# Kernel optimization log

Measured on AMD Instinct MI355X. Metric: run time of the kernel, lower is better.

## Reference

```python
import jax, jax.numpy as jnp
import numpy as np

B, N_PROP = 2, 512
C_FEAT, FH, FW = 256, 200, 200
NUM_CLASSES, NUM_STAGES = 81, 3
POOL, SR, SCALE = 7, 2, 0.25
IMG_H, IMG_W = 800.0, 800.0
FC_DIM = 1024
IN_DIM = C_FEAT * POOL * POOL
STDS = ((0.1, 0.1, 0.2, 0.2), (0.05, 0.05, 0.1, 0.1), (0.033, 0.033, 0.067, 0.067))
CLIP_VAL = float(np.log(1000.0 / 16))
SCORE_T, NMS_T, DETS, PRE_NMS = 0.05, 0.5, 100, 2048


def bilinear(f, y, x):
    # f: [C,H,W]; y,x: [M] sample coords (torchvision roi_align bilinear rules)
    H, W = f.shape[1], f.shape[2]
    valid = (y > -1.0) & (y < H) & (x > -1.0) & (x < W)
    y = jnp.clip(y, 0.0, H - 1.0)
    x = jnp.clip(x, 0.0, W - 1.0)
    y0 = jnp.floor(y).astype(jnp.int32)
    x0 = jnp.floor(x).astype(jnp.int32)
    y1 = jnp.minimum(y0 + 1, H - 1)
    x1 = jnp.minimum(x0 + 1, W - 1)
    ly, lx = y - y0, x - x0
    hy, hx = 1.0 - ly, 1.0 - lx
    v = (hy * hx) * f[:, y0, x0] + (hy * lx) * f[:, y0, x1] \
      + (ly * hx) * f[:, y1, x0] + (ly * lx) * f[:, y1, x1]
    return v * valid  # [C,M]


def roi_align(f, rois):
    # f: [C,H,W], rois: [N,4] image coords -> [N,C,POOL,POOL]
    b = rois * SCALE
    x1, y1, x2, y2 = b[:, 0], b[:, 1], b[:, 2], b[:, 3]
    rw = jnp.maximum(x2 - x1, 1.0)
    rh = jnp.maximum(y2 - y1, 1.0)
    bw, bh = rw / POOL, rh / POOL
    p = jnp.arange(POOL, dtype=f.dtype)
    s = (jnp.arange(SR, dtype=f.dtype) + 0.5) / SR
    gy = y1[:, None, None] + (p[None, :, None] + s[None, None, :]) * bh[:, None, None]  # [N,P,SR]
    gx = x1[:, None, None] + (p[None, :, None] + s[None, None, :]) * bw[:, None, None]
    n = rois.shape[0]
    yy = jnp.broadcast_to(gy[:, :, :, None, None], (n, POOL, SR, POOL, SR))
    xx = jnp.broadcast_to(gx[:, None, None, :, :], (n, POOL, SR, POOL, SR))
    vals = bilinear(f, yy.reshape(-1), xx.reshape(-1))  # [C, N*P*SR*P*SR]
    vals = vals.reshape(f.shape[0], n, POOL, SR, POOL, SR).mean(axis=(3, 5))
    return vals.transpose(1, 0, 2, 3)


def decode_clip(props, deltas, stds):
    px1, py1, px2, py2 = props[:, 0], props[:, 1], props[:, 2], props[:, 3]
    pw = jnp.maximum(px2 - px1, 1e-6)
    ph = jnp.maximum(py2 - py1, 1e-6)
    px = px1 + 0.5 * pw
    py = py1 + 0.5 * ph
    wx, wy, ww, wh = stds
    dx = deltas[:, 0] * wx
    dy = deltas[:, 1] * wy
    dw = jnp.minimum(deltas[:, 2] * ww, CLIP_VAL)
    dh = jnp.minimum(deltas[:, 3] * wh, CLIP_VAL)
    gx = dx * pw + px
    gy = dy * ph + py
    gw = jnp.exp(dw) * pw
    gh = jnp.exp(dh) * ph
    return jnp.stack([jnp.clip(gx - 0.5 * gw, 0.0, IMG_W),
                      jnp.clip(gy - 0.5 * gh, 0.0, IMG_H),
                      jnp.clip(gx + 0.5 * gw, 0.0, IMG_W),
                      jnp.clip(gy + 0.5 * gh, 0.0, IMG_H)], axis=1)


def box_iou(a, b):
    area_a = (a[:, 2] - a[:, 0]) * (a[:, 3] - a[:, 1])
    area_b = (b[:, 2] - b[:, 0]) * (b[:, 3] - b[:, 1])
    lt = jnp.maximum(a[:, None, :2], b[None, :, :2])
    rb = jnp.minimum(a[:, None, 2:], b[None, :, 2:])
    wh = jnp.maximum(rb - lt, 0.0)
    inter = wh[..., 0] * wh[..., 1]
    return inter / (area_a[:, None] + area_b[None, :] - inter + 1e-12)


def postprocess(boxes, probs):
    # boxes [N,4], probs [N,NUM_CLASSES] -> fixed-size padded detections
    n = boxes.shape[0]
    ws = boxes[:, 2] - boxes[:, 0]
    hs = boxes[:, 3] - boxes[:, 1]
    ok = (ws >= 1.0) & (hs >= 1.0)  # remove_small_boxes(min_size=1.0)
    fg = probs[:, 1:]               # drop background (class 0)
    sc = jnp.where((fg > SCORE_T) & ok[:, None], fg, -1.0).reshape(-1)  # [N*(C-1)]
    labels = jnp.broadcast_to(jnp.arange(1, NUM_CLASSES, dtype=jnp.int32)[None, :],
                              (n, NUM_CLASSES - 1)).reshape(-1)
    bflat = jnp.broadcast_to(boxes[:, None, :], (n, NUM_CLASSES - 1, 4)).reshape(-1, 4)
    vals, idx = jax.lax.top_k(sc, PRE_NMS)  # fixed-size candidate cap, sorted desc
    bsel = bflat[idx]
    lsel = labels[idx]
    # batched_nms trick: offset boxes per label so classes never overlap
    off = bsel + (lsel.astype(bsel.dtype) * (jnp.max(bsel) + 1.0))[:, None]
    iou = box_iou(off, off)
    valid = vals > 0.0
    ar = jnp.arange(PRE_NMS)
    def body(i, keep):
        sup = (iou[i] > NMS_T) & keep[i]
        return keep & ~(sup & (ar > i))
    keep = jax.lax.fori_loop(0, PRE_NMS, body, valid)
    order = jnp.argsort(jnp.where(keep, ar, PRE_NMS + ar))[:DETS]  # kept first, score order
    kv = keep[order]
    out_boxes = jnp.where(kv[:, None], bsel[order], 0.0)
    out_scores = jnp.where(kv, vals[order], 0.0)
    out_labels = jnp.where(kv, lsel[order], 0)
    return out_boxes, out_scores, out_labels


def cascade_forward(features, proposals, W1, b1, W2, b2, Wc, bc, Wr, br):
    cur = proposals  # [B,N,4]
    logits = None
    for s in range(NUM_STAGES):
        pooled = jax.vmap(roi_align)(features, cur)  # [B,N,C,P,P]
        x = pooled.reshape(B * N_PROP, IN_DIM)
        h = jax.nn.relu(x @ W1[s] + b1[s])
        h = jax.nn.relu(h @ W2[s] + b2[s])
        logits = h @ Wc[s] + bc[s]
        deltas = (h @ Wr[s] + br[s]).reshape(B, N_PROP, 4)
        stds = STDS[s]
        cur = jax.vmap(lambda p, d: decode_clip(p, d, stds))(cur, deltas)
    probs = jax.nn.softmax(logits, axis=-1).reshape(B, N_PROP, NUM_CLASSES)
    return jax.vmap(postprocess)(cur, probs)


def setup_inputs() -> dict:
    key = jax.random.key(0)
    ks = jax.random.split(key, 12)
    features = jax.random.normal(ks[0], (B, C_FEAT, FH, FW), jnp.float32)
    cx = jax.random.uniform(ks[1], (B, N_PROP), minval=0.0, maxval=IMG_W)
    cy = jax.random.uniform(ks[2], (B, N_PROP), minval=0.0, maxval=IMG_H)
    w = jax.random.uniform(ks[3], (B, N_PROP), minval=16.0, maxval=256.0)
    h = jax.random.uniform(ks[4], (B, N_PROP), minval=16.0, maxval=256.0)
    proposals = jnp.stack([jnp.clip(cx - w / 2, 0.0, IMG_W), jnp.clip(cy - h / 2, 0.0, IMG_H),
                           jnp.clip(cx + w / 2, 0.0, IMG_W), jnp.clip(cy + h / 2, 0.0, IMG_H)],
                          axis=-1)
    def lin(k, fan_in, shape):
        return jax.random.normal(k, shape, jnp.float32) / np.sqrt(fan_in).astype(np.float32)
    W1 = lin(ks[5], IN_DIM, (NUM_STAGES, IN_DIM, FC_DIM))
    W2 = lin(ks[6], FC_DIM, (NUM_STAGES, FC_DIM, FC_DIM))
    Wc = lin(ks[7], FC_DIM, (NUM_STAGES, FC_DIM, NUM_CLASSES))
    Wr = lin(ks[8], FC_DIM, (NUM_STAGES, FC_DIM, 4)) * 0.5
    b1 = jnp.zeros((NUM_STAGES, FC_DIM), jnp.float32)
    b2 = jnp.zeros((NUM_STAGES, FC_DIM), jnp.float32)
    bc = jnp.zeros((NUM_STAGES, NUM_CLASSES), jnp.float32)
    br = jnp.zeros((NUM_STAGES, 4), jnp.float32)
    return {"features": features, "proposals": proposals, "W1": W1, "b1": b1,
            "W2": W2, "b2": b2, "Wc": Wc, "bc": bc, "Wr": Wr, "br": br}


def reference(features, proposals, W1, b1, W2, b2, Wc, bc, Wr, br):
    return cascade_forward(features, proposals, W1, b1, W2, b2, Wc, bc, Wr, br)
```

## Files before the change

### kernel.cpp

```cpp
#include <hip/hip_runtime.h>
#include <float.h>
#include <math.h>

#define NB 2
#define NPROP 512
#define NROI 1024
#define CFEAT 256
#define FH 200
#define FW 200
#define HWSZ 40000
#define INDIM 12544
#define FCD 1024
#define NCLS 81
#define NCAND 40960
#define CAP 4096
#define NSEL 2048
#define DETS 100
#define CLIPV 4.135166556742356f

#define KKT1 392
#define KKT2 32
#define SPLITK 8

typedef __attribute__((ext_vector_type(8))) short short8v;
typedef __attribute__((ext_vector_type(8))) unsigned short ushort8v;
typedef __attribute__((ext_vector_type(4))) float float4v;

__device__ __forceinline__ unsigned short f2bf(float x) {
    unsigned u = __float_as_uint(x);
    unsigned r = (u + 0x7fffu + ((u >> 16) & 1u)) >> 16;
    return (unsigned short)r;
}
__device__ __forceinline__ float bf2f(unsigned short b) {
    return __uint_as_float(((unsigned)b) << 16);
}
__device__ __forceinline__ void split3(float x, unsigned short& h, unsigned short& m, unsigned short& l) {
    h = f2bf(x);
    float r1 = x - bf2f(h);
    m = f2bf(r1);
    float r2 = r1 - bf2f(m);
    l = f2bf(r2);
}

__device__ __forceinline__ void gload_lds16(const void* g, void* l) {
    __builtin_amdgcn_global_load_lds((const __attribute__((address_space(1))) unsigned int*)g,
                                     (__attribute__((address_space(3))) unsigned int*)l, 16, 0, 0);
}

__device__ __forceinline__ int swz8k(int o) {
    return o ^ ((((o >> 6) ^ (o >> 8)) & 3) << 4);
}

__global__ void zero_ints_k(int* p, int n) {
    int i = blockIdx.x * blockDim.x + threadIdx.x;
    if (i < n) p[i] = 0;
}

__global__ __launch_bounds__(256) void transpose_k(const float* __restrict__ in, float* __restrict__ out) {
    __shared__ float tile[32][33];
    int b = blockIdx.z;
    int hw0 = blockIdx.x * 32;
    int c0 = blockIdx.y * 32;
    int tx = threadIdx.x;
    int ty = threadIdx.y;
#pragma unroll
    for (int i = 0; i < 32; i += 8)
        tile[ty + i][tx] = in[((size_t)(b * CFEAT + c0 + ty + i)) * HWSZ + hw0 + tx];
    __syncthreads();
#pragma unroll
    for (int i = 0; i < 32; i += 8)
        out[((size_t)b * HWSZ + hw0 + ty + i) * CFEAT + c0 + tx] = tile[tx][ty + i];
}

template<bool TRANS>
__device__ __forceinline__ float bil_sample(const float* __restrict__ feat, int b, int c,
                                            float yy, float xx) {
    bool valid = (yy > -1.f) && (yy < (float)FH) && (xx > -1.f) && (xx < (float)FW);
    float yc = fminf(fmaxf(yy, 0.f), (float)(FH - 1));
    float xc = fminf(fmaxf(xx, 0.f), (float)(FW - 1));
    int y0 = (int)floorf(yc), x0 = (int)floorf(xc);
    int y1i = min(y0 + 1, FH - 1), x1i = min(x0 + 1, FW - 1);
    float ly = yc - (float)y0, lx = xc - (float)x0;
    float hy = 1.f - ly, hx = 1.f - lx;
    float v00, v01, v10, v11;
    if (TRANS) {
        const float* base = feat + (size_t)b * HWSZ * CFEAT;
        v00 = base[((size_t)(y0 * FW + x0)) * CFEAT + c];
        v01 = base[((size_t)(y0 * FW + x1i)) * CFEAT + c];
        v10 = base[((size_t)(y1i * FW + x0)) * CFEAT + c];
        v11 = base[((size_t)(y1i * FW + x1i)) * CFEAT + c];
    } else {
        const float* base = feat + ((size_t)(b * CFEAT + c)) * HWSZ;
        v00 = base[y0 * FW + x0];
        v01 = base[y0 * FW + x1i];
        v10 = base[y1i * FW + x0];
        v11 = base[y1i * FW + x1i];
    }
    float v = hy * hx * v00 + hy * lx * v01 + ly * hx * v10 + ly * lx * v11;
    return valid ? v : 0.f;
}

template<bool TRANS>
__global__ __launch_bounds__(256) void roi_k(const float* __restrict__ feat,
                                             const float* __restrict__ boxes,
                                             float* __restrict__ xout) {
    int pp = blockIdx.x, r = blockIdx.y, c = threadIdx.x;
    int b = r >> 9;
    const float* bx = boxes + (size_t)r * 4;
    float x1 = bx[0] * 0.25f, y1 = bx[1] * 0.25f, x2 = bx[2] * 0.25f, y2 = bx[3] * 0.25f;
    float rw = fmaxf(x2 - x1, 1.0f), rh = fmaxf(y2 - y1, 1.0f);
    float bw = rw / 7.0f, bh = rh / 7.0f;
    int py = pp / 7, px = pp % 7;
    float acc = 0.f;
#pragma unroll
    for (int sy = 0; sy < 2; ++sy)
#pragma unroll
        for (int sx = 0; sx < 2; ++sx)
            acc += bil_sample<TRANS>(feat, b, c,
                                     y1 + ((float)py + 0.25f + 0.5f * (float)sy) * bh,
                                     x1 + ((float)px + 0.25f + 0.5f * (float)sx) * bw);
    xout[(size_t)r * INDIM + pp * 256 + c] = acc * 0.25f;
}

__global__ __launch_bounds__(256) void roi_split4_k(const float* __restrict__ feat,
                                                    const float* __restrict__ boxes,
                                                    unsigned short* __restrict__ Ap) {
    int tid = threadIdx.x;
    int g = tid >> 7;
    int binhalf = (tid >> 6) & 1;
    int cl = tid & 63;
    int r = blockIdx.x * 2 + g;
    int b = r >> 9;
    const float* bx = boxes + (size_t)r * 4;
    float x1 = bx[0] * 0.25f, y1 = bx[1] * 0.25f, x2 = bx[2] * 0.25f, y2 = bx[3] * 0.25f;
    float rw = fmaxf(x2 - x1, 1.0f), rh = fmaxf(y2 - y1, 1.0f);
    float bw = rw / 7.0f, bh = rh / 7.0f;
    int mt = r >> 7, rr = r & 127;
    size_t pstr = (size_t)8 * KKT1 * 4096;
    const float* base = feat + (size_t)b * HWSZ * CFEAT;
    for (int pp = binhalf; pp < 49; pp += 2) {
        int py = pp / 7, px = pp % 7;
        float ax = 0.f, ay = 0.f, az = 0.f, aw = 0.f;
#pragma unroll
        for (int sy = 0; sy < 2; ++sy) {
#pragma unroll
            for (int sx = 0; sx < 2; ++sx) {
                float yy = y1 + ((float)py + 0.25f + 0.5f * (float)sy) * bh;
                float xx = x1 + ((float)px + 0.25f + 0.5f * (float)sx) * bw;
                bool valid = (yy > -1.f) && (yy < (float)FH) && (xx > -1.f) && (xx < (float)FW);
                float yc = fminf(fmaxf(yy, 0.f), (float)(FH - 1));
                float xc = fminf(fmaxf(xx, 0.f), (float)(FW - 1));
                int y0 = (int)floorf(yc), x0 = (int)floorf(xc);
                int y1i = min(y0 + 1, FH - 1), x1i = min(x0 + 1, FW - 1);
                float ly = yc - (float)y0, lx = xc - (float)x0;
                float hy = 1.f - ly, hx = 1.f - lx;
                float w00 = hy * hx, w01 = hy * lx, w10 = ly * hx, w11 = ly * lx;
                if (!valid) { w00 = w01 = w10 = w11 = 0.f; }
                float4 v00 = ((const float4*)(base + (size_t)(y0 * FW + x0) * CFEAT))[cl];
                float4 v01 = ((const float4*)(base + (size_t)(y0 * FW + x1i) * CFEAT))[cl];
                float4 v10 = ((const float4*)(base + (size_t)(y1i * FW + x0) * CFEAT))[cl];
                float4 v11 = ((const float4*)(base + (size_t)(y1i * FW + x1i) * CFEAT))[cl];
                ax += w00 * v00.x + w01 * v01.x + w10 * v10.x + w11 * v11.x;
                ay += w00 * v00.y + w01 * v01.y + w10 * v10.y + w11 * v11.y;
                az += w00 * v00.z + w01 * v01.z + w10 * v10.z + w11 * v11.z;
                aw += w00 * v00.w + w01 * v01.w + w10 * v10.w + w11 * v11.w;
            }
        }
        ax *= 0.25f; ay *= 0.25f; az *= 0.25f; aw *= 0.25f;
        ushort4 h4, m4, l4;
        split3(ax, h4.x, m4.x, l4.x);
        split3(ay, h4.y, m4.y, l4.y);
        split3(az, h4.z, m4.z, l4.z);
        split3(aw, h4.w, m4.w, l4.w);
        int k0 = pp * 256 + cl * 4;
        int kk = k0 >> 5;
        size_t tile = ((size_t)mt * KKT1 + kk) * 4096 + rr * 32 + (k0 & 31);
        *(ushort4*)&Ap[tile] = h4;
        *(ushort4*)&Ap[tile + pstr] = m4;
        *(ushort4*)&Ap[tile + 2 * pstr] = l4;
    }
}

template<bool PERM>
__global__ __launch_bounds__(256) void wsplit_k(const float* __restrict__ W,
                                                unsigned short* __restrict__ out, int kkT) {
    __shared__ float tf[32][132];
    int nt = blockIdx.x, kk = blockIdx.y;
    int t = threadIdx.x;
    int kloc = t >> 3;
    int f4 = t & 7;
    int krow;
    if (PERM) krow = ((kk & 7) * 32 + kloc) * 49 + (kk >> 3);
    else krow = kk * 32 + kloc;
    const float* src = W + (size_t)krow * 1024 + nt * 128;
#pragma unroll
    for (int q = 0; q < 4; ++q) {
        float4 v = *(const float4*)(src + (f4 + q * 8) * 4);
        *(float4*)&tf[kloc][(f4 + q * 8) * 4] = v;
    }
    __syncthreads();
    int r = t >> 1;
    size_t tileBase = ((size_t)nt * kkT + kk) * 4096;
    size_t pstr = (size_t)8 * kkT * 4096;
#pragma unroll
    for (int cc = 0; cc < 2; ++cc) {
        int c = (t & 1) * 2 + cc;
        ushort8v hv, mv, lv;
#pragma unroll
        for (int e = 0; e < 8; ++e) {
            unsigned short h, m, l;
            split3(tf[c * 8 + e][r], h, m, l);
            hv[e] = h; mv[e] = m; lv[e] = l;
        }
        size_t o = tileBase + r * 32 + c * 8;
        *(ushort8v*)&out[o] = hv;
        *(ushort8v*)&out[o + pstr] = mv;
        *(ushort8v*)&out[o + 2 * pstr] = lv;
    }
}

__global__ __launch_bounds__(256) void wsplit_head_k(const float* __restrict__ Wc,
                                                     const float* __restrict__ Wr,
                                                     unsigned short* __restrict__ out) {
    int kk = blockIdx.x, t = threadIdx.x;
    int r = t >> 1;
    int k0 = (t & 1) * 16;
    size_t pstr = (size_t)KKT2 * 4096;
    for (int e = 0; e < 16; ++e) {
        int k = k0 + e;
        int krow = kk * 32 + k;
        float v = 0.f;
        if (r < 81) v = Wc[(size_t)krow * 81 + r];
        else if (r < 85) v = Wr[(size_t)krow * 4 + (r - 81)];
        unsigned short h, m, l;
        split3(v, h, m, l);
        size_t o = (size_t)kk * 4096 + r * 32 + k;
        out[o] = h;
        out[o + pstr] = m;
        out[o + 2 * pstr] = l;
    }
}

#define TERM16(AF) { _Pragma("unroll") for (int i = 0; i < 4; ++i) _Pragma("unroll") \
    for (int j = 0; j < 4; ++j) acc[i][j] = __builtin_amdgcn_mfma_f32_16x16x32_bf16(AF[i], bf[j], acc[i][j], 0, 0, 0); }

__global__ __launch_bounds__(256) void gemm_mfma_k(const unsigned short* __restrict__ Ap,
                                                   const unsigned short* __restrict__ Bp,
                                                   float* __restrict__ partial,
                                                   int kkT, int kkPer, int NT, int N) {
    __shared__ unsigned short sA[3][4096];
    __shared__ unsigned short sB[2][3][4096];
    int tid = threadIdx.x;
    int phys = blockIdx.x;
    int logical = (phys & 7) * (gridDim.x >> 3) + (phys >> 3);
    int tpc = 8 * NT;
    int xy = logical % tpc;
    int ck = logical / tpc;
    int mt = xy & 7, nt = xy >> 3;
    int kk0 = ck * kkPer;
    size_t pstrA = (size_t)8 * kkT * 4096 * 2;
    size_t pstrB = (size_t)NT * kkT * 4096 * 2;
    const char* aBase = (const char*)(Ap + (size_t)mt * kkT * 4096);
    const char* bBase = (const char*)(Bp + (size_t)nt * kkT * 4096);

    float4v acc[4][4];
#pragma unroll
    for (int i = 0; i < 4; ++i)
#pragma unroll
        for (int j = 0; j < 4; ++j) acc[i][j] = (float4v){0.f, 0.f, 0.f, 0.f};

    int lane = tid & 63, wv = tid >> 6;
    int wr = wv >> 1, wc = wv & 1;
    int ln = lane & 15;
    int q = lane >> 4;
    int qs = (q ^ (ln ^ (ln >> 2))) & 3;
    int aoffE = (wr * 64 + ln) * 32 + qs * 8;
    int boffE = (wc * 64 + ln) * 32 + qs * 8;

    int o0 = tid * 16;
    int o1 = o0 + 4096;
    int s0 = swz8k(o0);
    int s1 = swz8k(o1);

    auto stageA = [&](int kk) {
        const char* at = aBase + (size_t)kk * 8192;
#pragma unroll
        for (int p = 0; p < 3; ++p) {
            gload_lds16(at + (size_t)p * pstrA + s0, (char*)sA[p] + o0);
            gload_lds16(at + (size_t)p * pstrA + s1, (char*)sA[p] + o1);
        }
    };
    auto stageB = [&](int buf, int kk) {
        const char* bt = bBase + (size_t)kk * 8192;
#pragma unroll
        for (int p = 0; p < 3; ++p) {
            gload_lds16(bt + (size_t)p * pstrB + s0, (char*)sB[buf][p] + o0);
            gload_lds16(bt + (size_t)p * pstrB + s1, (char*)sB[buf][p] + o1);
        }
    };

    stageB(0, kk0);
    for (int it = 0; it < kkPer; ++it) {
        int cur = it & 1;
        stageA(kk0 + it);
        if (it + 1 < kkPer) {
            stageB(cur ^ 1, kk0 + it + 1);
            asm volatile("s_waitcnt vmcnt(6)" ::: "memory");
        } else {
            asm volatile("s_waitcnt vmcnt(0)" ::: "memory");
        }
        __builtin_amdgcn_s_barrier();
        __builtin_amdgcn_sched_barrier(0);
        short8v af[3][4];
#pragma unroll
        for (int p = 0; p < 3; ++p)
#pragma unroll
            for (int f = 0; f < 4; ++f)
                af[p][f] = *(const short8v*)&sA[p][aoffE + f * 512];
        short8v bf[4];
#pragma unroll
        for (int f = 0; f < 4; ++f) bf[f] = *(const short8v*)&sB[cur][0][boffE + f * 512];
        TERM16(af[0]); TERM16(af[1]); TERM16(af[2]);
#pragma unroll
        for (int f = 0; f < 4; ++f) bf[f] = *(const short8v*)&sB[cur][1][boffE + f * 512];
        TERM16(af[0]); TERM16(af[1]);
#pragma unroll
        for (int f = 0; f < 4; ++f) bf[f] = *(const short8v*)&sB[cur][2][boffE + f * 512];
        TERM16(af[0]);
        __builtin_amdgcn_sched_barrier(0);
        __builtin_amdgcn_s_barrier();
    }
    float* outp = partial + (size_t)ck * 1024 * N;
    int row0 = mt * 128 + wr * 64 + (lane >> 4) * 4;
    int col = nt * 128 + wc * 64 + ln;
#pragma unroll
    for (int i = 0; i < 4; ++i)
#pragma unroll
        for (int j = 0; j < 4; ++j)
#pragma unroll
            for (int qq = 0; qq < 4; ++qq)
                outp[(size_t)(row0 + i * 16 + qq) * N + col + j * 16] = acc[i][j][qq];
}

template<int NS>
__global__ void reduce8_k(const float* __restrict__ partial, const float* __restrict__ bias,
                          unsigned short* __restrict__ planes) {
    int i = blockIdx.x * 256 + threadIdx.x;
    float s = 0.f;
#pragma unroll
    for (int c = 0; c < NS; ++c) s += partial[((size_t)c << 20) + i];
    s += bias[i & 1023];
    s = fmaxf(s, 0.f);
    int m = i >> 10, n = i & 1023;
    int mt = m >> 7, rr = m & 127, kk = n >> 5;
    unsigned short h, mm_, l;
    split3(s, h, mm_, l);
    size_t tile = ((size_t)mt * KKT2 + kk) * 4096 + rr * 32 + (n & 31);
    size_t pstr = (size_t)8 * KKT2 * 4096;
    planes[tile] = h;
    planes[tile + pstr] = mm_;
    planes[tile + 2 * pstr] = l;
}

__global__ __launch_bounds__(128) void head_dec_k(const float* __restrict__ partial,
                                                  const float* __restrict__ bc,
                                                  const float* __restrict__ br,
                                                  const float* __restrict__ prev,
                                                  float* __restrict__ logits,
                                                  float* __restrict__ nxt,
                                                  float wx, float wy, float ww, float wh,
                                                  int write_logits) {
    int m = blockIdx.x;
    int tid = threadIdx.x;
    __shared__ float dl[4];
    if (tid < 85) {
        float s = 0.f;
#pragma unroll
        for (int c = 0; c < 8; ++c) s += partial[(size_t)c * 131072 + m * 128 + tid];
        if (tid < 81) {
            if (write_logits) logits[(size_t)m * NCLS + tid] = s + bc[tid];
        } else {
            dl[tid - 81] = s + br[tid - 81];
        }
    }
    __syncthreads();
    if (tid == 0) {
        const float* p = prev + (size_t)m * 4;
        float px1 = p[0], py1 = p[1], px2 = p[2], py2 = p[3];
        float pw = fmaxf(px2 - px1, 1e-6f), ph = fmaxf(py2 - py1, 1e-6f);
        float pcx = px1 + 0.5f * pw, pcy = py1 + 0.5f * ph;
        float dx = dl[0] * wx, dy = dl[1] * wy;
        float dw = fminf(dl[2] * ww, CLIPV);
        float dh = fminf(dl[3] * wh, CLIPV);
        float gx = dx * pw + pcx, gy = dy * ph + pcy;
        float gw = expf(dw) * pw, gh = expf(dh) * ph;
        nxt[(size_t)m * 4 + 0] = fminf(fmaxf(gx - 0.5f * gw, 0.f), 800.f);
        nxt[(size_t)m * 4 + 1] = fminf(fmaxf(gy - 0.5f * gh, 0.f), 800.f);
        nxt[(size_t)m * 4 + 2] = fminf(fmaxf(gx + 0.5f * gw, 0.f), 800.f);
        nxt[(size_t)m * 4 + 3] = fminf(fmaxf(gy + 0.5f * gh, 0.f), 800.f);
    }
}

template<bool PERM>
__global__ __launch_bounds__(256) void gemm_k(const float* __restrict__ A,
                                              const float* __restrict__ Bm,
                                              float* __restrict__ partial,
                                              int K_total, int Kchunk) {
    const int M = 1024, N = 1024;
    __shared__ float As[2][16][128];
    __shared__ float Bs[2][16][64];
    int tid = threadIdx.x;
    int mb = blockIdx.x & 7;
    int nb = blockIdx.x >> 3;
    int ck = blockIdx.y;
    int k0 = ck * Kchunk;
    int am = tid >> 1;
    int ak = (tid & 1) * 8;
    int bk = tid >> 4;
    int bn = (tid & 15) * 4;
    int ty = tid >> 4, tx = tid & 15;
    const float* Aptr = A + (size_t)(mb * 128 + am) * K_total + k0 + ak;

    float acc[8][4];
#pragma unroll
    for (int i = 0; i < 8; ++i)
#pragma unroll
        for (int j = 0; j < 4; ++j) acc[i][j] = 0.f;

    auto bRowPtr = [&](int kk) -> const float* {
        int row = PERM ? ((kk & 255) * 49 + (kk >> 8)) : kk;
        return Bm + (size_t)row * N + nb * 64 + bn;
    };

    int T = Kchunk / 16;
    float4 a0 = *(const float4*)(Aptr);
    float4 a1 = *(const float4*)(Aptr + 4);
    float4 b0 = *(const float4*)bRowPtr(k0 + bk);
    As[0][ak + 0][am] = a0.x; As[0][ak + 1][am] = a0.y; As[0][ak + 2][am] = a0.z; As[0][ak + 3][am] = a0.w;
    As[0][ak + 4][am] = a1.x; As[0][ak + 5][am] = a1.y; As[0][ak + 6][am] = a1.z; As[0][ak + 7][am] = a1.w;
    *(float4*)&Bs[0][bk][bn] = b0;
    __syncthreads();

    int p = 0;
    for (int t = 0; t < T; ++t) {
        if (t + 1 < T) {
            a0 = *(const float4*)(Aptr + (t + 1) * 16);
            a1 = *(const float4*)(Aptr + (t + 1) * 16 + 4);
            b0 = *(const float4*)bRowPtr(k0 + (t + 1) * 16 + bk);
        }
#pragma unroll
        for (int k = 0; k < 16; ++k) {
            float4 av0 = *(const float4*)&As[p][k][ty * 8];
            float4 av1 = *(const float4*)&As[p][k][ty * 8 + 4];
            float4 bv = *(const float4*)&Bs[p][k][tx * 4];
            float ar[8] = {av0.x, av0.y, av0.z, av0.w, av1.x, av1.y, av1.z, av1.w};
            float br_[4] = {bv.x, bv.y, bv.z, bv.w};
#pragma unroll
            for (int i = 0; i < 8; ++i)
#pragma unroll
                for (int j = 0; j < 4; ++j) acc[i][j] = fmaf(ar[i], br_[j], acc[i][j]);
        }
        if (t + 1 < T) {
            __syncthreads();
            int qb = 1 - p;
            As[qb][ak + 0][am] = a0.x; As[qb][ak + 1][am] = a0.y; As[qb][ak + 2][am] = a0.z; As[qb][ak + 3][am] = a0.w;
            As[qb][ak + 4][am] = a1.x; As[qb][ak + 5][am] = a1.y; As[qb][ak + 6][am] = a1.z; As[qb][ak + 7][am] = a1.w;
            *(float4*)&Bs[qb][bk][bn] = b0;
            __syncthreads();
            p = qb;
        }
    }
    float* out = partial + ((size_t)ck * M + mb * 128 + ty * 8) * N + nb * 64 + tx * 4;
#pragma unroll
    for (int i = 0; i < 8; ++i) {
        float4 v = make_float4(acc[i][0], acc[i][1], acc[i][2], acc[i][3]);
        *(float4*)(out + (size_t)i * N) = v;
    }
}

__global__ void reduce4_k(const float* __restrict__ partial, const float* __restrict__ bias,
                          float* __restrict__ out) {
    const int MN = 1024 * 1024;
    int i = blockIdx.x * 256 + threadIdx.x;
    if (i >= MN) return;
    float s = partial[i] + partial[(size_t)MN + i] + partial[(size_t)2 * MN + i] + partial[(size_t)3 * MN + i];
    s += bias[i & 1023];
    out[i] = fmaxf(s, 0.f);
}

__global__ __launch_bounds__(128) void head_k(const float* __restrict__ h,
                                              const float* __restrict__ Wc, const float* __restrict__ bc,
                                              const float* __restrict__ Wr, const float* __restrict__ br,
                                              float* __restrict__ logits, float* __restrict__ deltas,
                                              int write_logits) {
    __shared__ float hs[1024];
    int m = blockIdx.x;
    int tid = threadIdx.x;
    const float4* hp = (const float4*)(h + (size_t)m * 1024);
    ((float4*)hs)[tid] = hp[tid];
    ((float4*)hs)[tid + 128] = hp[tid + 128];
    __syncthreads();
    int j = tid;
    if (j < 85) {
        bool is_cls = j < 81;
        const float* Wp = is_cls ? Wc : Wr;
        int stride = is_cls ? 81 : 4;
        int col = is_cls ? j : j - 81;
        float s0 = 0.f, s1 = 0.f, s2 = 0.f, s3 = 0.f;
        for (int k = 0; k < 1024; k += 4) {
            s0 = fmaf(hs[k + 0], Wp[(k + 0) * stride + col], s0);
            s1 = fmaf(hs[k + 1], Wp[(k + 1) * stride + col], s1);
            s2 = fmaf(hs[k + 2], Wp[(k + 2) * stride + col], s2);
            s3 = fmaf(hs[k + 3], Wp[(k + 3) * stride + col], s3);
        }
        float s = (s0 + s1) + (s2 + s3);
        if (is_cls) {
            if (write_logits) logits[(size_t)m * NCLS + col] = s + bc[col];
        } else {
            deltas[(size_t)m * 4 + col] = s + br[col];
        }
    }
}

__global__ void decode_k(const float* __restrict__ prev, const float* __restrict__ deltas,
                         float* __restrict__ nxt, float wx, float wy, float ww, float wh) {
    int r = blockIdx.x * 256 + threadIdx.x;
    if (r >= NROI) return;
    const float* p = prev + (size_t)r * 4;
    const float* d = deltas + (size_t)r * 4;
    float px1 = p[0], py1 = p[1], px2 = p[2], py2 = p[3];
    float pw = fmaxf(px2 - px1, 1e-6f), ph = fmaxf(py2 - py1, 1e-6f);
    float pcx = px1 + 0.5f * pw, pcy = py1 + 0.5f * ph;
    float dx = d[0] * wx, dy = d[1] * wy;
    float dw = fminf(d[2] * ww, CLIPV);
    float dh = fminf(d[3] * wh, CLIPV);
    float gx = dx * pw + pcx, gy = dy * ph + pcy;
    float gw = expf(dw) * pw, gh = expf(dh) * ph;
    nxt[(size_t)r * 4 + 0] = fminf(fmaxf(gx - 0.5f * gw, 0.f), 800.f);
    nxt[(size_t)r * 4 + 1] = fminf(fmaxf(gy - 0.5f * gh, 0.f), 800.f);
    nxt[(size_t)r * 4 + 2] = fminf(fmaxf(gx + 0.5f * gw, 0.f), 800.f);
    nxt[(size_t)r * 4 + 3] = fminf(fmaxf(gy + 0.5f * gh, 0.f), 800.f);
}

__global__ __launch_bounds__(128) void softmax_build_k(const float* __restrict__ logits,
                                                       const float* __restrict__ boxes,
                                                       float* __restrict__ sc,
                                                       int* __restrict__ vcount) {
    __shared__ float red[128];
    int m = blockIdx.x;
    int b = m >> 9, rr = m & 511;
    int tid = threadIdx.x;
    float v = (tid < NCLS) ? logits[(size_t)m * NCLS + tid] : -FLT_MAX;
    red[tid] = v;
    __syncthreads();
    for (int o = 64; o; o >>= 1) {
        if (tid < o) red[tid] = fmaxf(red[tid], red[tid + o]);
        __syncthreads();
    }
    float mx = red[0];
    __syncthreads();
    float e = (tid < NCLS) ? expf(v - mx) : 0.f;
    red[tid] = e;
    __syncthreads();
    for (int o = 64; o; o >>= 1) {
        if (tid < o) red[tid] += red[tid + o];
        __syncthreads();
    }
    float ssum = red[0];
    const float* bx = boxes + (size_t)m * 4;
    bool ok = (bx[2] - bx[0] >= 1.f) && (bx[3] - bx[1] >= 1.f);
    if (tid >= 1 && tid < NCLS) {
        float p = e / ssum;
        float sval = (p > 0.05f && ok) ? p : -1.0f;
        sc[(size_t)b * NCAND + rr * 80 + (tid - 1)] = sval;
        if (sval > 0.f) atomicAdd(&vcount[b], 1);
    }
}

__global__ __launch_bounds__(1024) void find_pivot_k(const float* __restrict__ sc,
                                                     const int* __restrict__ vcount,
                                                     float* __restrict__ pivot) {
    int b = blockIdx.x;
    const float* s = sc + (size_t)b * NCAND;
    __shared__ int tot;
    int V = vcount[b];
    if (V <= CAP) {
        if (threadIdx.x == 0) pivot[b] = 0.f;
        return;
    }
    float v[40];
#pragma unroll
    for (int i = 0; i < 40; ++i) v[i] = s[threadIdx.x + i * 1024];
    unsigned u = 0;
    for (int bit = 30; bit >= 0; --bit) {
        unsigned cand = u | (1u << bit);
        float cf = __uint_as_float(cand);
        if (threadIdx.x == 0) tot = 0;
        __syncthreads();
        int cnt = 0;
#pragma unroll
        for (int i = 0; i < 40; ++i) cnt += (v[i] >= cf) ? 1 : 0;
        for (int o = 32; o; o >>= 1) cnt += __shfl_down(cnt, o);
        if ((threadIdx.x & 63) == 0) atomicAdd(&tot, cnt);
        __syncthreads();
        if (tot >= NSEL) u = cand;
        __syncthreads();
    }
    if (threadIdx.x == 0) pivot[b] = __uint_as_float(u);
}

__global__ void compact_k(const float* __restrict__ sc, const float* __restrict__ pivot,
                          float* __restrict__ ckey, int* __restrict__ cidx, int* __restrict__ ccount) {
    int f = blockIdx.x * 256 + threadIdx.x;
    if (f >= NB * NCAND) return;
    int b = f / NCAND, ff = f % NCAND;
    float s = sc[f];
    float pv = pivot[b];
    if (s > 0.f && s >= pv) {
        int slot = atomicAdd(&ccount[b], 1);
        if (slot < CAP) {
            ckey[(size_t)b * CAP + slot] = s;
            cidx[(size_t)b * CAP + slot] = ff;
        }
    }
}

__global__ __launch_bounds__(1024) void sort_select_k(const float* __restrict__ ckey,
                                                      const int* __restrict__ cidx,
                                                      const int* __restrict__ ccount,
                                                      const float* __restrict__ boxes,
                                                      float* __restrict__ selb, float* __restrict__ seloff,
                                                      float* __restrict__ selsc, int* __restrict__ sellab,
                                                      unsigned long long* __restrict__ vmask) {
    int b = blockIdx.x;
    __shared__ float ks[CAP];
    __shared__ int is[CAP];
    __shared__ float rmax[1024];
    int cnt = min(ccount[b], CAP);
    for (int i = threadIdx.x; i < CAP; i += 1024) {
        if (i < cnt) {
            ks[i] = ckey[(size_t)b * CAP + i];
            is[i] = cidx[(size_t)b * CAP + i];
        } else {
            ks[i] = -FLT_MAX;
            is[i] = 0x7FFFFFFF;
        }
    }
    __syncthreads();
    for (int k = 2; k <= CAP; k <<= 1) {
        for (int j = k >> 1; j > 0; j >>= 1) {
            for (int t = threadIdx.x; t < CAP; t += 1024) {
                int l = t ^ j;
                if (l > t) {
                    bool up = ((t & k) == 0);
                    float a = ks[t], bb = ks[l];
                    int ia = is[t], ib = is[l];
                    bool a_first = (a > bb) || (a == bb && ia < ib);
                    bool doswap = up ? !a_first : a_first;
                    if (doswap) {
                        ks[t] = bb; ks[l] = a;
                        is[t] = ib; is[l] = ia;
                    }
                }
            }
            __syncthreads();
        }
    }
    float lm = -FLT_MAX;
    for (int i = threadIdx.x; i < NSEL; i += 1024) {
        if (ks[i] > 0.f) {
            const float* bb = boxes + (size_t)(b * NPROP + is[i] / 80) * 4;
            lm = fmaxf(lm, fmaxf(fmaxf(bb[0], bb[1]), fmaxf(bb[2], bb[3])));
        }
    }
    rmax[threadIdx.x] = lm;
    __syncthreads();
    for (int o = 512; o; o >>= 1) {
        if (threadIdx.x < o) rmax[threadIdx.x] = fmaxf(rmax[threadIdx.x], rmax[threadIdx.x + o]);
        __syncthreads();
    }
    float maxb = (rmax[0] > -FLT_MAX) ? rmax[0] : 0.f;
    __syncthreads();
    for (int pass = 0; pass < 2; ++pass) {
        int i = pass * 1024 + threadIdx.x;
        bool v = ks[i] > 0.f;
        int idx = is[i];
        int rr = idx / 80;
        int cls = idx % 80 + 1;
        float b0 = 0.f, b1 = 0.f, b2 = 0.f, b3 = 0.f, offv = 0.f;
        if (v) {
            const float* bb = boxes + (size_t)(b * NPROP + rr) * 4;
            b0 = bb[0]; b1 = bb[1]; b2 = bb[2]; b3 = bb[3];
            offv = (maxb + 1.f) * (float)cls;
        }
        float* sb = selb + ((size_t)b * NSEL + i) * 4;
        sb[0] = b0; sb[1] = b1; sb[2] = b2; sb[3] = b3;
        float* so = seloff + ((size_t)b * NSEL + i) * 4;
        so[0] = b0 + offv; so[1] = b1 + offv; so[2] = b2 + offv; so[3] = b3 + offv;
        selsc[(size_t)b * NSEL + i] = v ? ks[i] : 0.f;
        sellab[(size_t)b * NSEL + i] = cls;
        unsigned long long m = __ballot(v);
        if ((threadIdx.x & 63) == 0) vmask[b * 32 + pass * 16 + (threadIdx.x >> 6)] = m;
    }
}

__global__ __launch_bounds__(256) void sup_k(const float* __restrict__ seloff,
                                             const float* __restrict__ selsc,
                                             unsigned long long* __restrict__ sup) {
    int b = blockIdx.y;
    int wave = threadIdx.x >> 6;
    int lane = threadIdx.x & 63;
    int pair = blockIdx.x * 4 + wave;
    int i = pair >> 5;
    int w = pair & 31;
    int j = w * 64 + lane;
    unsigned long long m = 0;
    if (w >= (i >> 6) && selsc[(size_t)b * NSEL + i] > 0.f) {
        const float* oi = seloff + ((size_t)b * NSEL + i) * 4;
        const float* oj = seloff + ((size_t)b * NSEL + j) * 4;
        float ax1 = oi[0], ay1 = oi[1], ax2 = oi[2], ay2 = oi[3];
        float bx1 = oj[0], by1 = oj[1], bx2 = oj[2], by2 = oj[3];
        float areaA = (ax2 - ax1) * (ay2 - ay1);
        float areaB = (bx2 - bx1) * (by2 - by1);
        float ltx = fmaxf(ax1, bx1), lty = fmaxf(ay1, by1);
        float rbx = fminf(ax2, bx2), rby = fminf(ay2, by2);
        float iw = fmaxf(rbx - ltx, 0.f), ih = fmaxf(rby - lty, 0.f);
        float inter = iw * ih;
        float iou = inter / (areaA + areaB - inter + 1e-12f);
        m = __ballot(iou > 0.5f);
    }
    if (lane == 0) sup[((size_t)b * NSEL + i) * 32 + w] = m;
}

__global__ __launch_bounds__(256) void nms_scan_k(const unsigned long long* __restrict__ vmask,
                                                  const unsigned long long* __restrict__ sup,
                                                  const float* __restrict__ selb,
                                                  const float* __restrict__ selsc,
                                                  const int* __restrict__ sellab,
                                                  float* __restrict__ out) {
    int b = blockIdx.x;
    __shared__ unsigned long long keepw[32];
    __shared__ int pref[33];
    int tid = threadIdx.x;
    if (tid < 64) {
        int lane = tid;
        unsigned long long kw = (lane < 32) ? vmask[b * 32 + lane] : 0ull;
        const unsigned long long* supB = sup + (size_t)b * NSEL * 32;
        int kept = 0;
        for (int w = 0; w < 32; ++w) {
            unsigned long long cur = __shfl(kw, w);
            if (cur) {
                unsigned long long R = supB[(size_t)(w * 64 + lane) * 32 + w];
                for (int b0 = 0; b0 < 64; b0 += 8) {
                    unsigned long long r0 = __shfl(R, b0 + 0);
                    unsigned long long r1 = __shfl(R, b0 + 1);
                    unsigned long long r2 = __shfl(R, b0 + 2);
                    unsigned long long r3 = __shfl(R, b0 + 3);
                    unsigned long long r4 = __shfl(R, b0 + 4);
                    unsigned long long r5 = __shfl(R, b0 + 5);
                    unsigned long long r6 = __shfl(R, b0 + 6);
                    unsigned long long r7 = __shfl(R, b0 + 7);
                    unsigned long long hi;
#define NMS_STEP(rr_, dd_) { int bb = b0 + dd_; \
                    hi = (bb == 63) ? 0ull : (~0ull << (bb + 1)); \
                    cur &= ~((0ull - ((cur >> bb) & 1ull)) & rr_ & hi); }
                    NMS_STEP(r0, 0) NMS_STEP(r1, 1) NMS_STEP(r2, 2) NMS_STEP(r3, 3)
                    NMS_STEP(r4, 4) NMS_STEP(r5, 5) NMS_STEP(r6, 6) NMS_STEP(r7, 7)
#undef NMS_STEP
                }
                kept += __popcll(cur);
                if (lane == w) kw = cur;
                if (kept >= DETS) break;
                int v = lane & 31;
                int h = lane >> 5;
                unsigned long long acc = 0;
                const unsigned long long* rowb = supB + (size_t)(w * 64 + h) * 32 + v;
#pragma unroll 8
                for (int t = 0; t < 32; ++t) {
                    unsigned long long msk = 0ull - ((cur >> (h + 2 * t)) & 1ull);
                    acc |= rowb[(size_t)(2 * t) * 32] & msk;
                }
                acc |= __shfl_xor(acc, 32);
                if (lane < 32 && lane > w) kw &= ~acc;
            }
        }
        if (lane < 32) keepw[lane] = kw;
    }
    __syncthreads();
    if (tid == 0) {
        int s = 0;
        for (int w = 0; w < 32; ++w) { pref[w] = s; s += __popcll(keepw[w]); }
        pref[32] = s;
    }
    __syncthreads();
    for (int i = tid; i < 600; i += 256) {
        if (i < 400) out[b * 400 + i] = 0.f;
        else if (i < 500) out[800 + b * 100 + (i - 400)] = 0.f;
        else out[1000 + b * 100 + (i - 500)] = 0.f;
    }
    __syncthreads();
    for (int e = tid; e < NSEL; e += 256) {
        int w = e >> 6;
        unsigned long long kw = keepw[w];
        if ((kw >> (e & 63)) & 1ull) {
            int rank = pref[w] + __popcll(kw & ((1ull << (e & 63)) - 1ull));
            if (rank < DETS) {
                const float* sb = selb + ((size_t)b * NSEL + e) * 4;
                out[b * 400 + rank * 4 + 0] = sb[0];
                out[b * 400 + rank * 4 + 1] = sb[1];
                out[b * 400 + rank * 4 + 2] = sb[2];
                out[b * 400 + rank * 4 + 3] = sb[3];
                out[800 + b * 100 + rank] = selsc[(size_t)b * NSEL + e];
                out[1000 + b * 100 + rank] = (float)sellab[(size_t)b * NSEL + e];
            }
        }
    }
}

extern "C" void kernel_launch(void* const* d_in, const int* in_sizes, int n_in,
                              void* d_out, int out_size, void* d_ws, size_t ws_size,
                              hipStream_t stream) {
    const float* features = (const float*)d_in[0];
    const float* proposals = (const float*)d_in[1];
    const float* W1 = (const float*)d_in[2];
    const float* b1 = (const float*)d_in[3];
    const float* W2 = (const float*)d_in[4];
    const float* b2 = (const float*)d_in[5];
    const float* Wc = (const float*)d_in[6];
    const float* bc = (const float*)d_in[7];
    const float* Wr = (const float*)d_in[8];
    const float* br = (const float*)d_in[9];

    char* ws = (char*)d_ws;
    size_t off = 0;
    auto alloc = [&](size_t bytes) -> void* {
        void* p = ws + off;
        off += (bytes + 255) & ~(size_t)255;
        return p;
    };

    float* logits = (float*)alloc((size_t)NROI * NCLS * 4);
    float* deltas = (float*)alloc((size_t)NROI * 4 * 4);
    float* cur1 = (float*)alloc((size_t)NROI * 4 * 4);
    float* cur2 = (float*)alloc((size_t)NROI * 4 * 4);
    float* cur3 = (float*)alloc((size_t)NROI * 4 * 4);
    float* sc = (float*)alloc((size_t)NB * NCAND * 4);
    float* ckey = (float*)alloc((size_t)NB * CAP * 4);
    int* cidx = (int*)alloc((size_t)NB * CAP * 4);
    int* counters = (int*)alloc(256);
    float* pivot = (float*)(counters + 4);
    float* selb = (float*)alloc((size_t)NB * NSEL * 4 * 4);
    float* seloff = (float*)alloc((size_t)NB * NSEL * 4 * 4);
    float* selsc = (float*)alloc((size_t)NB * NSEL * 4);
    int* sellab = (int*)alloc((size_t)NB * NSEL * 4);
    unsigned long long* vmask = (unsigned long long*)alloc((size_t)NB * 32 * 8);
    unsigned long long* sup = (unsigned long long*)alloc((size_t)NB * NSEL * 32 * 8);

    const float stds[3][4] = {{0.1f, 0.1f, 0.2f, 0.2f},
                              {0.05f, 0.05f, 0.1f, 0.1f},
                              {0.033f, 0.033f, 0.067f, 0.067f}};
    float* curbufs[3] = {cur1, cur2, cur3};
    const float* curp = proposals;

    size_t planes1 = (size_t)3 * 8 * KKT1 * 4096 * 2;
    size_t planes2 = (size_t)3 * 8 * KKT2 * 4096 * 2;
    size_t planesH = (size_t)3 * 1 * KKT2 * 4096 * 2;
    size_t mfma_need = planes1 * 2 + planes2 * 3 + planesH +
                       (size_t)SPLITK * (1 << 20) * 4 +
                       (size_t)NB * HWSZ * CFEAT * 4 + 65536;

    zero_ints_k<<<1, 64, 0, stream>>>(counters, 4);

    if (off + mfma_need <= ws_size) {
        unsigned short* Ap1 = (unsigned short*)alloc(planes1);
        unsigned short* Bp1 = (unsigned short*)alloc(planes1);
        unsigned short* h1p = (unsigned short*)alloc(planes2);
        unsigned short* W2Tp = (unsigned short*)alloc(planes2);
        unsigned short* h2p = (unsigned short*)alloc(planes2);
        unsigned short* Whp = (unsigned short*)alloc(planesH);
        float* partial = (float*)alloc((size_t)SPLITK * (1 << 20) * 4);
        float* featT = (float*)alloc((size_t)NB * HWSZ * CFEAT * 4);

        transpose_k<<<dim3(1250, 8, 2), dim3(32, 8), 0, stream>>>(features, featT);

        for (int s = 0; s < 3; ++s) {
            roi_split4_k<<<dim3(NROI / 2), 256, 0, stream>>>(featT, curp, Ap1);
            wsplit_k<true><<<dim3(8, KKT1), 256, 0, stream>>>(W1 + (size_t)s * INDIM * FCD, Bp1, KKT1);
            gemm_mfma_k<<<dim3(64 * SPLITK), 256, 0, stream>>>(Ap1, Bp1, partial, KKT1, KKT1 / SPLITK, 8, 1024);
            reduce8_k<SPLITK><<<4096, 256, 0, stream>>>(partial, b1 + s * FCD, h1p);
            wsplit_k<false><<<dim3(8, KKT2), 256, 0, stream>>>(W2 + (size_t)s * FCD * FCD, W2Tp, KKT2);
            gemm_mfma_k<<<dim3(512), 256, 0, stream>>>(h1p, W2Tp, partial, KKT2, 4, 8, 1024);
            reduce8_k<8><<<4096, 256, 0, stream>>>(partial, b2 + s * FCD, h2p);
            wsplit_head_k<<<dim3(KKT2), 256, 0, stream>>>(Wc + (size_t)s * FCD * NCLS,
                                                          Wr + (size_t)s * FCD * 4, Whp);
            gemm_mfma_k<<<dim3(64), 256, 0, stream>>>(h2p, Whp, partial, KKT2, 4, 1, 128);
            head_dec_k<<<dim3(NROI), 128, 0, stream>>>(partial, bc + s * NCLS, br + s * 4,
                                                       curp, logits, curbufs[s],
                                                       stds[s][0], stds[s][1], stds[s][2], stds[s][3],
                                                       (s == 2) ? 1 : 0);
            curp = curbufs[s];
        }
    } else {
        float* x = (float*)alloc((size_t)NROI * INDIM * 4);
        float* partial = (float*)alloc((size_t)4 * 1024 * 1024 * 4);
        float* h1 = (float*)alloc((size_t)NROI * FCD * 4);
        float* h2 = (float*)alloc((size_t)NROI * FCD * 4);
        float* featT = (float*)alloc((size_t)NB * HWSZ * CFEAT * 4);
        bool use_trans = (off <= ws_size);

        if (use_trans)
            transpose_k<<<dim3(1250, 8, 2), dim3(32, 8), 0, stream>>>(features, featT);

        for (int s = 0; s < 3; ++s) {
            if (use_trans)
                roi_k<true><<<dim3(49, 1024), 256, 0, stream>>>(featT, curp, x);
            else
                roi_k<false><<<dim3(49, 1024), 256, 0, stream>>>(features, curp, x);
            gemm_k<true><<<dim3(128, 4), 256, 0, stream>>>(x, W1 + (size_t)s * INDIM * FCD, partial, INDIM, 3136);
            reduce4_k<<<4096, 256, 0, stream>>>(partial, b1 + s * FCD, h1);
            gemm_k<false><<<dim3(128, 4), 256, 0, stream>>>(h1, W2 + (size_t)s * FCD * FCD, partial, FCD, 256);
            reduce4_k<<<4096, 256, 0, stream>>>(partial, b2 + s * FCD, h2);
            head_k<<<1024, 128, 0, stream>>>(h2, Wc + (size_t)s * FCD * NCLS, bc + s * NCLS,
                                             Wr + (size_t)s * FCD * 4, br + s * 4,
                                             logits, deltas, (s == 2) ? 1 : 0);
            decode_k<<<4, 256, 0, stream>>>(curp, deltas, curbufs[s],
                                            stds[s][0], stds[s][1], stds[s][2], stds[s][3]);
            curp = curbufs[s];
        }
    }

    softmax_build_k<<<dim3(NROI), 128, 0, stream>>>(logits, curp, sc, counters);
    find_pivot_k<<<2, 1024, 0, stream>>>(sc, counters, pivot);
    compact_k<<<320, 256, 0, stream>>>(sc, pivot, ckey, cidx, counters + 2);
    sort_select_k<<<2, 1024, 0, stream>>>(ckey, cidx, counters + 2, curp, selb, seloff, selsc, sellab, vmask);
    sup_k<<<dim3(16384, 2), 256, 0, stream>>>(seloff, selsc, sup);
    nms_scan_k<<<2, 256, 0, stream>>>(vmask, sup, selb, selsc, sellab, (float*)d_out);
}
```

Baseline: 1.035 ms.

## Halve GEMM N-tile to 64 and double-buffer A alongside B

The split-bf16 MFMA GEMM output tile shrinks from 128x128 to 128x64. Each of the four waves now owns a 32-row strip across all 64 columns, and the grid doubles so more workgroups run at once. A and B tiles are now both double-buffered in one combined stage step that prefetches the next K slice, with the wait count adjusted to match. This trades more global A traffic and less reuse per tile for more parallelism and better load/compute overlap.

```diff
diff --git a/kernel.cpp b/kernel.cpp
--- a/kernel.cpp
+++ b/kernel.cpp
@@ -241,15 +241,15 @@
     }
 }
 
-#define TERM16(AF) { _Pragma("unroll") for (int i = 0; i < 4; ++i) _Pragma("unroll") \
+#define TERM8(AF) { _Pragma("unroll") for (int i = 0; i < 2; ++i) _Pragma("unroll") \
     for (int j = 0; j < 4; ++j) acc[i][j] = __builtin_amdgcn_mfma_f32_16x16x32_bf16(AF[i], bf[j], acc[i][j], 0, 0, 0); }
 
 __global__ __launch_bounds__(256) void gemm_mfma_k(const unsigned short* __restrict__ Ap,
                                                    const unsigned short* __restrict__ Bp,
                                                    float* __restrict__ partial,
                                                    int kkT, int kkPer, int NT, int N) {
-    __shared__ unsigned short sA[3][4096];
-    __shared__ unsigned short sB[2][3][4096];
+    __shared__ unsigned short sA[2][3][4096];
+    __shared__ unsigned short sB[2][3][2048];
     int tid = threadIdx.x;
     int phys = blockIdx.x;
     int logical = (phys & 7) * (gridDim.x >> 3) + (phys >> 3);
@@ -259,82 +259,74 @@
     int mt = xy & 7, nt = xy >> 3;
     int kk0 = ck * kkPer;
     size_t pstrA = (size_t)8 * kkT * 4096 * 2;
-    size_t pstrB = (size_t)NT * kkT * 4096 * 2;
+    size_t pstrB = (size_t)(NT >> 1) * kkT * 4096 * 2;
     const char* aBase = (const char*)(Ap + (size_t)mt * kkT * 4096);
-    const char* bBase = (const char*)(Bp + (size_t)nt * kkT * 4096);
-
-    float4v acc[4][4];
-#pragma unroll
-    for (int i = 0; i < 4; ++i)
+    const char* bBase = (const char*)Bp + ((size_t)(nt >> 1) * kkT * 4096 + (size_t)(nt & 1) * 2048) * 2;
+
+    float4v acc[2][4];
+#pragma unroll
+    for (int i = 0; i < 2; ++i)
 #pragma unroll
         for (int j = 0; j < 4; ++j) acc[i][j] = (float4v){0.f, 0.f, 0.f, 0.f};
 
     int lane = tid & 63, wv = tid >> 6;
-    int wr = wv >> 1, wc = wv & 1;
     int ln = lane & 15;
     int q = lane >> 4;
     int qs = (q ^ (ln ^ (ln >> 2))) & 3;
-    int aoffE = (wr * 64 + ln) * 32 + qs * 8;
-    int boffE = (wc * 64 + ln) * 32 + qs * 8;
+    int aoffE = (wv * 32 + ln) * 32 + qs * 8;
+    int boffE = ln * 32 + qs * 8;
 
     int o0 = tid * 16;
     int o1 = o0 + 4096;
     int s0 = swz8k(o0);
     int s1 = swz8k(o1);
 
-    auto stageA = [&](int kk) {
-        const char* at = aBase + (size_t)kk * 8192;
+    auto stage = [&](int buf, int kk) {
 #pragma unroll
         for (int p = 0; p < 3; ++p) {
-            gload_lds16(at + (size_t)p * pstrA + s0, (char*)sA[p] + o0);
-            gload_lds16(at + (size_t)p * pstrA + s1, (char*)sA[p] + o1);
+            const char* at = aBase + (size_t)p * pstrA + (size_t)kk * 8192;
+            gload_lds16(at + s0, (char*)sA[buf][p] + o0);
+            gload_lds16(at + s1, (char*)sA[buf][p] + o1);
+            const char* bt = bBase + (size_t)p * pstrB + (size_t)kk * 8192;
+            gload_lds16(bt + s0, (char*)sB[buf][p] + o0);
         }
     };
-    auto stageB = [&](int buf, int kk) {
-        const char* bt = bBase + (size_t)kk * 8192;
-#pragma unroll
-        for (int p = 0; p < 3; ++p) {
-            gload_lds16(bt + (size_t)p * pstrB + s0, (char*)sB[buf][p] + o0);
-            gload_lds16(bt + (size_t)p * pstrB + s1, (char*)sB[buf][p] + o1);
-        }
-    };
-
-    stageB(0, kk0);
+
+    stage(0, kk0);
     for (int it = 0; it < kkPer; ++it) {
         int cur = it & 1;
-        stageA(kk0 + it);
         if (it + 1 < kkPer) {
-            stageB(cur ^ 1, kk0 + it + 1);
-            asm volatile("s_waitcnt vmcnt(6)" ::: "memory");
+            stage(cur ^ 1, kk0 + it + 1);
+            asm volatile("s_waitcnt vmcnt(9)" ::: "memory");
         } else {
             asm volatile("s_waitcnt vmcnt(0)" ::: "memory");
         }
         __builtin_amdgcn_s_barrier();
         __builtin_amdgcn_sched_barrier(0);
-        short8v af[3][4];
+        short8v af[3][2];
 #pragma unroll
         for (int p = 0; p < 3; ++p)
 #pragma unroll
-            for (int f = 0; f < 4; ++f)
-                af[p][f] = *(const short8v*)&sA[p][aoffE + f * 512];
+            for (int f = 0; f < 2; ++f)
+                af[p][f] = *(const short8v*)&sA[cur][p][aoffE + f * 512];
         short8v bf[4];
 #pragma unroll
         for (int f = 0; f < 4; ++f) bf[f] = *(const short8v*)&sB[cur][0][boffE + f * 512];
-        TERM16(af[0]); TERM16(af[1]); TERM16(af[2]);
+        TERM8(af[0]); TERM8(af[1]); TERM8(af[2]);
 #pragma unroll
         for (int f = 0; f < 4; ++f) bf[f] = *(const short8v*)&sB[cur][1][boffE + f * 512];
-        TERM16(af[0]); TERM16(af[1]);
+        TERM8(af[0]); TERM8(af[1]);
 #pragma unroll
         for (int f = 0; f < 4; ++f) bf[f] = *(const short8v*)&sB[cur][2][boffE + f * 512];
-        TERM16(af[0]);
+        TERM8(af[0]);
         __builtin_amdgcn_sched_barrier(0);
         __builtin_amdgcn_s_barrier();
     }
     float* outp = partial + (size_t)ck * 1024 * N;
-    int row0 = mt * 128 + wr * 64 + (lane >> 4) * 4;
-    int col = nt * 128 + wc * 64 + ln;
-#pragma unroll
-    for (int i = 0; i < 4; ++i)
+    int row0 = mt * 128 + wv * 32 + (lane >> 4) * 4;
+    int col = nt * 64 + ln;
+#pragma unroll
+    for (int i = 0; i < 2; ++i)
 #pragma unroll
         for (int j = 0; j < 4; ++j)
 #pragma unroll
@@ -886,14 +878,14 @@
         for (int s = 0; s < 3; ++s) {
             roi_split4_k<<<dim3(NROI / 2), 256, 0, stream>>>(featT, curp, Ap1);
             wsplit_k<true><<<dim3(8, KKT1), 256, 0, stream>>>(W1 + (size_t)s * INDIM * FCD, Bp1, KKT1);
-            gemm_mfma_k<<<dim3(64 * SPLITK), 256, 0, stream>>>(Ap1, Bp1, partial, KKT1, KKT1 / SPLITK, 8, 1024);
+            gemm_mfma_k<<<dim3(1024), 256, 0, stream>>>(Ap1, Bp1, partial, KKT1, KKT1 / SPLITK, 16, 1024);
             reduce8_k<SPLITK><<<4096, 256, 0, stream>>>(partial, b1 + s * FCD, h1p);
             wsplit_k<false><<<dim3(8, KKT2), 256, 0, stream>>>(W2 + (size_t)s * FCD * FCD, W2Tp, KKT2);
-            gemm_mfma_k<<<dim3(512), 256, 0, stream>>>(h1p, W2Tp, partial, KKT2, 4, 8, 1024);
+            gemm_mfma_k<<<dim3(1024), 256, 0, stream>>>(h1p, W2Tp, partial, KKT2, 4, 16, 1024);
             reduce8_k<8><<<4096, 256, 0, stream>>>(partial, b2 + s * FCD, h2p);
             wsplit_head_k<<<dim3(KKT2), 256, 0, stream>>>(Wc + (size_t)s * FCD * NCLS,
                                                           Wr + (size_t)s * FCD * 4, Whp);
-            gemm_mfma_k<<<dim3(64), 256, 0, stream>>>(h2p, Whp, partial, KKT2, 4, 1, 128);
+            gemm_mfma_k<<<dim3(128), 256, 0, stream>>>(h2p, Whp, partial, KKT2, 4, 2, 128);
             head_dec_k<<<dim3(NROI), 128, 0, stream>>>(partial, bc + s * NCLS, br + s * 4,
                                                        curp, logits, curbufs[s],
                                                        stds[s][0], stds[s][1], stds[s][2], stds[s][3],
```

After: 1.137 ms. 1.1x slower.
